# Performance work log

Measured on AMD Instinct MI355X. Metric: run time of the kernel, lower is better.

The kernel has to match this reference:

```python
import jax, jax.numpy as jnp
import numpy as np

DIM = 512
NUM_HEADS = 8
HEAD_DIM = DIM // NUM_HEADS
MAX_SLICES = 1024
SCALE = float(np.sqrt(HEAD_DIM))


def setup_inputs() -> dict:
    key = jax.random.key(0)
    ks = jax.random.split(key, 12)
    B, Nv, Nt, D = 4, 1024, 512, DIM
    std = 0.02
    inp = {
        "visual_tokens": jax.random.normal(ks[0], (B, Nv, D), jnp.float32),
        "text_tokens": jax.random.normal(ks[1], (B, Nt, D), jnp.float32),
        # Linear weights stored as [in, out] (i.e., torch W^T), so y = x @ W + b
        "W_Q": jax.random.normal(ks[2], (D, D), jnp.float32) * std,
        "b_Q": jnp.zeros((D,), jnp.float32),
        "W_K": jax.random.normal(ks[3], (D, D), jnp.float32) * std,
        "b_K": jnp.zeros((D,), jnp.float32),
        "W_V": jax.random.normal(ks[4], (D, D), jnp.float32) * std,
        "b_V": jnp.zeros((D,), jnp.float32),
        "W_O": jax.random.normal(ks[5], (D, D), jnp.float32) * std,
        "b_O": jnp.zeros((D,), jnp.float32),
        "bias_table": jax.random.normal(ks[6], (2 * MAX_SLICES - 1, NUM_HEADS), jnp.float32) * std,
        "ln_gamma": jnp.ones((D,), jnp.float32),
        "ln_beta": jnp.zeros((D,), jnp.float32),
    }
    return inp


def _layernorm(x, gamma, beta, eps=1e-5):
    mu = jnp.mean(x, axis=-1, keepdims=True)
    var = jnp.var(x, axis=-1, keepdims=True)
    return (x - mu) * jax.lax.rsqrt(var + eps) * gamma + beta


def reference(visual_tokens, text_tokens, W_Q, b_Q, W_K, b_K, W_V, b_V, W_O, b_O,
              bias_table, ln_gamma, ln_beta):
    Z = jnp.concatenate([visual_tokens, text_tokens], axis=1)  # [B, N, D]
    B, N, D = Z.shape
    Z = _layernorm(Z, ln_gamma, ln_beta)

    def proj(W, b):
        return (Z @ W + b).reshape(B, N, NUM_HEADS, HEAD_DIM).transpose(0, 2, 1, 3)

    Q = proj(W_Q, b_Q)  # [B, H, N, hd]
    K = proj(W_K, b_K)
    V = proj(W_V, b_V)

    attn = jnp.einsum("bhqd,bhkd->bhqk", Q, K) / SCALE  # [B, H, N, N]

    # relative slice bias: [H, N, N]
    coords = jnp.arange(N)
    rel = coords[:, None] - coords[None, :] + (MAX_SLICES - 1)
    rel = jnp.clip(rel, 0, 2 * MAX_SLICES - 2)
    bias = bias_table[rel]                      # [N, N, H]
    bias = jnp.transpose(bias, (2, 0, 1))[None]  # [1, H, N, N]

    attn = jax.nn.softmax(attn + bias, axis=-1)
    out = jnp.einsum("bhqk,bhkd->bhqd", attn, V)  # [B, H, N, hd]
    out = out.transpose(0, 2, 1, 3).reshape(B, N, D)
    return out @ W_O + b_O
```

## Files before the change

kernel.cpp:

```cpp
#include <hip/hip_runtime.h>
#include <stdint.h>

#define NSEQ   1536
#define NBATCH 4
#define NM     (NBATCH * NSEQ)
#define DMODEL 512
#define NHEAD  8
#define HD     64
#define TBLN   2047

typedef __attribute__((ext_vector_type(4)))  float f32x4;
typedef __attribute__((ext_vector_type(16))) float f32x16;
typedef __attribute__((ext_vector_type(4)))  int   i32x4;
typedef __attribute__((ext_vector_type(2)))  unsigned u32x2;
typedef __attribute__((ext_vector_type(8)))  __bf16 bf16x8;
typedef unsigned short u16;

static_assert(sizeof(bf16x8) == 16, "bf16x8 must be 16B");

__device__ inline u16 f2bf(float f) {
  union { float f; uint32_t u; } v; v.f = f;
  uint32_t u = v.u;
  return (u16)((u + 0x7fffu + ((u >> 16) & 1u)) >> 16);
}

__device__ inline bf16x8 ld_bf8(const u16* p) {
  i32x4 v = *(const i32x4*)p;
  return __builtin_bit_cast(bf16x8, v);
}

__device__ inline f32x4 mfma16(bf16x8 a, bf16x8 b, f32x4 c) {
  return __builtin_amdgcn_mfma_f32_16x16x32_bf16(a, b, c, 0, 0, 0);
}

__device__ inline f32x16 mfma32(bf16x8 a, bf16x8 b, f32x16 c) {
  return __builtin_amdgcn_mfma_f32_32x32x16_bf16(a, b, c, 0, 0, 0);
}

__device__ inline void gload_lds16(const void* g, void* l) {
  __builtin_amdgcn_global_load_lds(
      (__attribute__((address_space(1))) void*)(g),
      (__attribute__((address_space(3))) void*)(l), 16, 0, 0);
}

__device__ inline uint32_t pkbf(float a, float b) {
  uint32_t r;
  asm("v_cvt_pk_bf16_f32 %0, %1, %2" : "=v"(r) : "v"(a), "v"(b));
  return r;
}

__device__ inline void plswap(uint32_t& a, uint32_t& b, int hi) {
#if __has_builtin(__builtin_amdgcn_permlane32_swap)
  u32x2 r = __builtin_amdgcn_permlane32_swap(a, b, false, false);
  a = r[0]; b = r[1];
#else
  const uint32_t as = (uint32_t)__shfl_xor((int)a, 32);
  const uint32_t bs = (uint32_t)__shfl_xor((int)b, 32);
  const uint32_t na = hi ? bs : a;
  const uint32_t nb = hi ? b : as;
  a = na; b = nb;
#endif
}

__device__ inline float exp2_raw(float x) {
  float r;
  asm("v_exp_f32 %0, %1" : "=v"(r) : "v"(x));
  return r;
}

__device__ inline float bfhi(uint32_t u) {
  union { uint32_t u; float f; } v; v.u = u & 0xffff0000u; return v.f;
}
__device__ inline float bflo(uint32_t u) {
  union { uint32_t u; float f; } v; v.u = u << 16; return v.f;
}

__global__ __launch_bounds__(256) void ln_kernel(
    const float* __restrict__ vis, const float* __restrict__ txt,
    const float* __restrict__ gamma, const float* __restrict__ beta,
    u16* __restrict__ zn) {
  const int lane = threadIdx.x & 63;
  const int row  = blockIdx.x * 4 + (threadIdx.x >> 6);
  const int b = row / NSEQ, n = row - b * NSEQ;
  const float* src = (n < 1024) ? (vis + ((size_t)b * 1024 + n) * DMODEL)
                                : (txt + ((size_t)b * 512 + (n - 1024)) * DMODEL);
  const float4* s4 = (const float4*)src;
  float4 x0 = s4[lane], x1 = s4[lane + 64];
  float s = x0.x + x0.y + x0.z + x0.w + x1.x + x1.y + x1.z + x1.w;
  float q = x0.x*x0.x + x0.y*x0.y + x0.z*x0.z + x0.w*x0.w
          + x1.x*x1.x + x1.y*x1.y + x1.z*x1.z + x1.w*x1.w;
  #pragma unroll
  for (int m = 1; m < 64; m <<= 1) { s += __shfl_xor(s, m); q += __shfl_xor(q, m); }
  const float mean = s * (1.0f / 512.0f);
  const float var  = q * (1.0f / 512.0f) - mean * mean;
  const float rstd = rsqrtf(var + 1e-5f);
  const float4* g4 = (const float4*)gamma;
  const float4* b4 = (const float4*)beta;
  float4 g0 = g4[lane], g1 = g4[lane + 64], p0 = b4[lane], p1 = b4[lane + 64];
  u16* dst = zn + (size_t)row * DMODEL;
  ushort4 o0, o1;
  o0.x = f2bf((x0.x - mean) * rstd * g0.x + p0.x);
  o0.y = f2bf((x0.y - mean) * rstd * g0.y + p0.y);
  o0.z = f2bf((x0.z - mean) * rstd * g0.z + p0.z);
  o0.w = f2bf((x0.w - mean) * rstd * g0.w + p0.w);
  o1.x = f2bf((x1.x - mean) * rstd * g1.x + p1.x);
  o1.y = f2bf((x1.y - mean) * rstd * g1.y + p1.y);
  o1.z = f2bf((x1.z - mean) * rstd * g1.z + p1.z);
  o1.w = f2bf((x1.w - mean) * rstd * g1.w + p1.w);
  *(ushort4*)(dst + lane * 4)        = o0;
  *(ushort4*)(dst + (lane + 64) * 4) = o1;
}

__global__ __launch_bounds__(256) void wtrans_kernel(
    const float* __restrict__ WQ, const float* __restrict__ WK,
    const float* __restrict__ WV, const float* __restrict__ WO,
    u16* __restrict__ wqkvt, u16* __restrict__ wot) {
  __shared__ float t[32][33];
  const int m = blockIdx.z;
  const float* W = (m == 0) ? WQ : (m == 1) ? WK : (m == 2) ? WV : WO;
  const int n0 = blockIdx.x * 32, k0 = blockIdx.y * 32;
  const int tx = threadIdx.x & 31, ty = threadIdx.x >> 5;
  #pragma unroll
  for (int j = 0; j < 4; ++j)
    t[ty + j * 8][tx] = W[(size_t)(k0 + ty + j * 8) * DMODEL + n0 + tx];
  __syncthreads();
  u16* out = (m < 3) ? (wqkvt + (size_t)m * DMODEL * DMODEL) : wot;
  #pragma unroll
  for (int j = 0; j < 4; ++j)
    out[(size_t)(n0 + ty + j * 8) * DMODEL + k0 + tx] = f2bf(t[tx][ty + j * 8]);
}

__global__ __launch_bounds__(256) void gemm_qkv(
    const u16* __restrict__ A, const u16* __restrict__ Bt,
    const float* __restrict__ bQ, const float* __restrict__ bK, const float* __restrict__ bV,
    u16* __restrict__ Q, u16* __restrict__ Kk, u16* __restrict__ Vt) {
  __shared__ __align__(16) u16 lat[128 * 64];
  __shared__ __align__(16) u16 lbt[96 * 64];
  const int tid = threadIdx.x, lane = tid & 63, w = tid >> 6;
  const int wr = w >> 1, wc = w & 1;
  const int m0 = blockIdx.y * 128, n0 = blockIdx.x * 96;
  f32x4 acc[4][3] = {};
  for (int kt = 0; kt < 8; ++kt) {
    const int k0 = kt * 64;
    #pragma unroll
    for (int i = 0; i < 4; ++i) {
      int ch = tid + 256 * i;
      int row = ch >> 3, pc = ch & 7;
      int kk = k0 + ((pc ^ (row & 7)) << 3);
      gload_lds16(A + (size_t)(m0 + row) * DMODEL + kk, lat + (size_t)ch * 8);
    }
    #pragma unroll
    for (int i = 0; i < 3; ++i) {
      int ch = tid + 256 * i;
      int row = ch >> 3, pc = ch & 7;
      int kk = k0 + ((pc ^ (row & 7)) << 3);
      gload_lds16(Bt + (size_t)(n0 + row) * DMODEL + kk, lbt + (size_t)ch * 8);
    }
    __syncthreads();
    #pragma unroll
    for (int ks = 0; ks < 2; ++ks) {
      bf16x8 af[4], bfr[3];
      const int cc = ks * 4 + (lane >> 4);
      #pragma unroll
      for (int f = 0; f < 4; ++f) {
        int ra = wr * 64 + f * 16 + (lane & 15);
        af[f]  = ld_bf8(lat + ra * 64 + ((cc ^ (ra & 7)) << 3));
      }
      #pragma unroll
      for (int f = 0; f < 3; ++f) {
        int rb = wc * 48 + f * 16 + (lane & 15);
        bfr[f] = ld_bf8(lbt + rb * 64 + ((cc ^ (rb & 7)) << 3));
      }
      #pragma unroll
      for (int fr = 0; fr < 4; ++fr)
        #pragma unroll
        for (int fc = 0; fc < 3; ++fc)
          acc[fr][fc] = mfma16(af[fr], bfr[fc], acc[fr][fc]);
    }
    __syncthreads();
  }
  #pragma unroll
  for (int fr = 0; fr < 4; ++fr) {
    const int mbase = m0 + wr * 64 + fr * 16 + ((lane >> 4) << 2);
    const int b = mbase / NSEQ;
    const int nseq = mbase - b * NSEQ;
    #pragma unroll
    for (int fc = 0; fc < 3; ++fc) {
      const int col = n0 + wc * 48 + fc * 16 + (lane & 15);
      const int which = col >> 9;
      const int cw = col & 511;
      const int h = cw >> 6, d = cw & 63;
      const float bias = (which == 0) ? bQ[cw] : (which == 1) ? bK[cw] : bV[cw];
      if (which < 2) {
        u16* dst = ((which == 0) ? Q : Kk) + ((size_t)(b * NHEAD + h) * NSEQ + nseq) * HD + d;
        #pragma unroll
        for (int r = 0; r < 4; ++r) dst[(size_t)r * HD] = f2bf(acc[fr][fc][r] + bias);
      } else {
        ushort4 pv;
        pv.x = f2bf(acc[fr][fc][0] + bias);
        pv.y = f2bf(acc[fr][fc][1] + bias);
        pv.z = f2bf(acc[fr][fc][2] + bias);
        pv.w = f2bf(acc[fr][fc][3] + bias);
        *(ushort4*)(Vt + ((size_t)(b * NHEAD + h) * HD + d) * NSEQ + nseq) = pv;
      }
    }
  }
}

__global__ __launch_bounds__(256) void gemm_oproj(
    const u16* __restrict__ A, const u16* __restrict__ Bt,
    const float* __restrict__ bO, float* __restrict__ out) {
  __shared__ __align__(16) u16 lat[64 * 64];
  __shared__ __align__(16) u16 lbt[64 * 64];
  const int tid = threadIdx.x, lane = tid & 63, w = tid >> 6;
  const int wr = w >> 1, wc = w & 1;
  const int m0 = blockIdx.y * 64, n0 = blockIdx.x * 64;
  f32x4 acc[2][2] = {};
  for (int kt = 0; kt < 8; ++kt) {
    const int k0 = kt * 64;
    #pragma unroll
    for (int i = 0; i < 2; ++i) {
      int ch = tid + 256 * i;
      int row = ch >> 3, pc = ch & 7;
      int kk = k0 + ((pc ^ (row & 7)) << 3);
      gload_lds16(A  + (size_t)(m0 + row) * DMODEL + kk, lat + (size_t)ch * 8);
      gload_lds16(Bt + (size_t)(n0 + row) * DMODEL + kk, lbt + (size_t)ch * 8);
    }
    __syncthreads();
    #pragma unroll
    for (int ks = 0; ks < 2; ++ks) {
      bf16x8 af[2], bfr[2];
      const int cc = ks * 4 + (lane >> 4);
      #pragma unroll
      for (int f = 0; f < 2; ++f) {
        int ra = wr * 32 + f * 16 + (lane & 15);
        af[f]  = ld_bf8(lat + ra * 64 + ((cc ^ (ra & 7)) << 3));
        int rb = wc * 32 + f * 16 + (lane & 15);
        bfr[f] = ld_bf8(lbt + rb * 64 + ((cc ^ (rb & 7)) << 3));
      }
      #pragma unroll
      for (int fr = 0; fr < 2; ++fr)
        #pragma unroll
        for (int fc = 0; fc < 2; ++fc)
          acc[fr][fc] = mfma16(af[fr], bfr[fc], acc[fr][fc]);
    }
    __syncthreads();
  }
  #pragma unroll
  for (int fr = 0; fr < 2; ++fr) {
    const int mbase = m0 + wr * 32 + fr * 16 + ((lane >> 4) << 2);
    #pragma unroll
    for (int fc = 0; fc < 2; ++fc) {
      const int col = n0 + wc * 32 + fc * 16 + (lane & 15);
      const float bias = bO[col];
      float* dst = out + (size_t)mbase * DMODEL + col;
      #pragma unroll
      for (int r = 0; r < 4; ++r) dst[(size_t)r * DMODEL] = acc[fr][fc][r] + bias;
    }
  }
}

__global__ __launch_bounds__(768, 3) void attn_kernel(
    const u16* __restrict__ Q, const u16* __restrict__ K,
    const u16* __restrict__ Vt, const float* __restrict__ table,
    u16* __restrict__ O) {
  __shared__ __align__(16) char smem[77824];
  u16* rb2k = (u16*)smem;
  const int tid = threadIdx.x, lane = tid & 63, w = tid >> 6;
  const int bid = blockIdx.x;
  const int xcd = bid & 7, idx = bid >> 3;
  const int bh  = xcd * 4 + (idx & 3);
  const int qt  = idx >> 2;
  const int h   = bh & (NHEAD - 1);
  for (int t = tid; t < 2 * 3072; t += 768) {
    const int c = (t >= 3072) ? 1 : 0;
    const int x = t - c * 3072;
    int src = 2558 - (x + c);
    src = src < 0 ? 0 : (src > 2046 ? 2046 : src);
    rb2k[c * 3072 + x] = f2bf(table[(size_t)src * NHEAD + h] * 1.4426950408889634f);
  }

  const int lo32 = lane & 31, hi = lane >> 5;
  const int ws = (w < 6) ? w : (w - 6);
  const int hf = (w < 6) ? 0 : 1;
  const int kbase = hf * 768;
  const int q  = qt * 192 + ws * 32 + lo32;
  const u16* Qb = Q  + (size_t)bh * NSEQ * HD;
  const u16* Kb = K  + (size_t)bh * NSEQ * HD;
  const u16* Vb = Vt + (size_t)bh * HD * NSEQ;

  const int tloc = tid - hf * 384;
  u16* kl0 = (u16*)(smem + 12288) + hf * 2 * 4096;
  u16* vl0 = (u16*)(smem + 45056) + hf * 2 * 4096;
#define STAGE(b, k0loc)                                                       \
  if (tloc < 256) {                                                           \
    _Pragma("unroll")                                                         \
    for (int i = 0; i < 2; ++i) {                                             \
      int ch = tloc + 256 * i;                                                \
      int row = ch >> 3, pc = ch & 7;                                         \
      int col = (pc ^ (row & 7)) << 3;                                        \
      gload_lds16(Kb + (size_t)(kbase + (k0loc) + row) * HD + col,            \
                  kl0 + (size_t)(b) * 4096 + ch * 8);                         \
      gload_lds16(Vb + (size_t)row * NSEQ + kbase + (k0loc) + col,            \
                  vl0 + (size_t)(b) * 4096 + ch * 8);                         \
    }                                                                         \
  }

  bf16x8 qf[4];
  #pragma unroll
  for (int ds = 0; ds < 4; ++ds)
    qf[ds] = ld_bf8(Qb + (size_t)q * HD + ds * 16 + hi * 8);

  float l_part = 0.f;
  f32x16 acc[2] = {};

  const int rswz = lo32 & 7;
  const int T0  = 1535 - q + 4 * hi + kbase;
  const int c2  = T0 & 1;
  const int dwb = (T0 - c2) >> 1;
  const uint32_t* rbp32 = (const uint32_t*)(rb2k + c2 * 3072);
  const float c1 = 0.125f * 1.4426950408889634f;

  STAGE(0, 0);
  __syncthreads();
  int cur = 0;

  for (int kt = 0; kt < 12; ++kt) {
    const int nxt = cur ^ 1;
    if (kt < 11) {
      STAGE(nxt, (kt + 1) * 64);
      asm volatile("s_waitcnt vmcnt(4)" ::: "memory");
    } else {
      asm volatile("s_waitcnt vmcnt(0)" ::: "memory");
    }
    __builtin_amdgcn_s_barrier();
    const u16* kb = (u16*)(smem + 12288) + (hf * 2 + cur) * 4096;
    const u16* vb = (u16*)(smem + 45056) + (hf * 2 + cur) * 4096;
    #pragma unroll
    for (int ktile = 0; ktile < 2; ++ktile) {
      f32x16 st = {};
      __builtin_amdgcn_s_setprio(1);
      #pragma unroll
      for (int ds = 0; ds < 4; ++ds) {
        const int row = ktile * 32 + lo32;
        const bf16x8 kf = ld_bf8(kb + row * 64 + (((2 * ds + hi) ^ rswz) << 3));
        st = mfma32(kf, qf[ds], st);
      }
      __builtin_amdgcn_s_setprio(0);
      const int dwk = dwb + ((kt * 64 + ktile * 32) >> 1);
      float bv[4][4];
      #pragma unroll
      for (int gp = 0; gp < 4; ++gp) {
        const uint32_t u0 = rbp32[dwk + 4 * gp];
        const uint32_t u1 = rbp32[dwk + 4 * gp + 1];
        bv[gp][0] = bflo(u0); bv[gp][1] = bfhi(u0);
        bv[gp][2] = bflo(u1); bv[gp][3] = bfhi(u1);
      }
      #pragma unroll
      for (int r = 0; r < 16; ++r) {
        float p = exp2_raw(__builtin_fmaf(st[r], c1, bv[r >> 2][r & 3]));
        st[r] = p;
        l_part += p;
      }
      uint32_t wv[8];
      #pragma unroll
      for (int i = 0; i < 8; ++i) wv[i] = pkbf(st[2 * i], st[2 * i + 1]);
      plswap(wv[0], wv[2], hi);  plswap(wv[1], wv[3], hi);
      plswap(wv[4], wv[6], hi);  plswap(wv[5], wv[7], hi);
      i32x4 b0; b0[0] = (int)wv[0]; b0[1] = (int)wv[1]; b0[2] = (int)wv[2]; b0[3] = (int)wv[3];
      i32x4 b1; b1[0] = (int)wv[4]; b1[1] = (int)wv[5]; b1[2] = (int)wv[6]; b1[3] = (int)wv[7];
      const bf16x8 pb0 = __builtin_bit_cast(bf16x8, b0);
      const bf16x8 pb1 = __builtin_bit_cast(bf16x8, b1);
      __builtin_amdgcn_s_setprio(1);
      #pragma unroll
      for (int dh = 0; dh < 2; ++dh) {
        const int vrow = dh * 32 + lo32;
        const bf16x8 va0 = ld_bf8(vb + vrow * 64 + (((4 * ktile + 0 + hi) ^ rswz) << 3));
        acc[dh] = mfma32(va0, pb0, acc[dh]);
        const bf16x8 va1 = ld_bf8(vb + vrow * 64 + (((4 * ktile + 2 + hi) ^ rswz) << 3));
        acc[dh] = mfma32(va1, pb1, acc[dh]);
      }
      __builtin_amdgcn_s_setprio(0);
    }
    __builtin_amdgcn_s_barrier();
    cur = nxt;
  }
  float* scr = (float*)(smem + 12288);
  if (hf == 1) {
    float* wb = scr + ws * 2112;
    #pragma unroll
    for (int dh = 0; dh < 2; ++dh)
      #pragma unroll
      for (int i = 0; i < 4; ++i) {
        f32x4 c4; c4[0] = acc[dh][4*i]; c4[1] = acc[dh][4*i+1];
        c4[2] = acc[dh][4*i+2]; c4[3] = acc[dh][4*i+3];
        ((f32x4*)wb)[(dh * 4 + i) * 64 + lane] = c4;
      }
    wb[2048 + lane] = l_part;
  }
  __syncthreads();
  if (hf == 0) {
    const float* rb = scr + ws * 2112;
    #pragma unroll
    for (int dh = 0; dh < 2; ++dh)
      #pragma unroll
      for (int i = 0; i < 4; ++i) {
        const f32x4 c4 = ((const f32x4*)rb)[(dh * 4 + i) * 64 + lane];
        acc[dh][4*i] += c4[0]; acc[dh][4*i+1] += c4[1];
        acc[dh][4*i+2] += c4[2]; acc[dh][4*i+3] += c4[3];
      }
    l_part += rb[2048 + lane];
    float l_r = l_part + __shfl_xor(l_part, 32);
    const float inv = 1.0f / l_r;
    const int b = bh >> 3;
    u16* orow = O + ((size_t)(b * NSEQ + q)) * DMODEL + h * HD;
    #pragma unroll
    for (int dh = 0; dh < 2; ++dh)
      #pragma unroll
      for (int gp = 0; gp < 4; ++gp) {
        uint2 o4;
        o4.x = pkbf(acc[dh][4*gp]   * inv, acc[dh][4*gp+1] * inv);
        o4.y = pkbf(acc[dh][4*gp+2] * inv, acc[dh][4*gp+3] * inv);
        *(uint2*)(orow + dh * 32 + 8 * gp + 4 * hi) = o4;
      }
  }
#undef STAGE
}

extern "C" void kernel_launch(void* const* d_in, const int* in_sizes, int n_in,
                              void* d_out, int out_size, void* d_ws, size_t ws_size,
                              hipStream_t stream) {
  const float* vis   = (const float*)d_in[0];
  const float* txt   = (const float*)d_in[1];
  const float* WQ    = (const float*)d_in[2];
  const float* bQ    = (const float*)d_in[3];
  const float* WK    = (const float*)d_in[4];
  const float* bK    = (const float*)d_in[5];
  const float* WV    = (const float*)d_in[6];
  const float* bV    = (const float*)d_in[7];
  const float* WO    = (const float*)d_in[8];
  const float* bO    = (const float*)d_in[9];
  const float* table = (const float*)d_in[10];
  const float* gamma = (const float*)d_in[11];
  const float* beta  = (const float*)d_in[12];
  float* out = (float*)d_out;

  char* p = (char*)d_ws;
  u16* zn    = (u16*)p; p += (size_t)NM * DMODEL * 2;
  u16* wqkvt = (u16*)p; p += (size_t)3 * DMODEL * DMODEL * 2;
  u16* wot   = (u16*)p; p += (size_t)DMODEL * DMODEL * 2;
  u16* q     = (u16*)p; p += (size_t)NM * DMODEL * 2;
  u16* k     = (u16*)p; p += (size_t)NM * DMODEL * 2;
  u16* vt    = (u16*)p; p += (size_t)NM * DMODEL * 2;
  u16* o     = (u16*)p; p += (size_t)NM * DMODEL * 2;

  hipLaunchKernelGGL(ln_kernel, dim3(NM / 4), dim3(256), 0, stream,
                     vis, txt, gamma, beta, zn);
  hipLaunchKernelGGL(wtrans_kernel, dim3(16, 16, 4), dim3(256), 0, stream,
                     WQ, WK, WV, WO, wqkvt, wot);
  hipLaunchKernelGGL(gemm_qkv, dim3(16, 48), dim3(256), 0, stream,
                     zn, wqkvt, bQ, bK, bV, q, k, vt);
  hipLaunchKernelGGL(attn_kernel, dim3(256), dim3(768), 0, stream,
                     q, k, vt, table, o);
  hipLaunchKernelGGL(gemm_oproj, dim3(8, 96), dim3(256), 0, stream,
                     o, wot, bO, out);
}
```

Baseline: 81.99 us.

## Double-buffer LDS in projection GEMMs with larger M tiles and MFMA priority

Both projection GEMMs (QKV and output) now keep two LDS stages, prefetching the next K tile while MFMAs run on the current one. They use partial vmcnt waits and raw barriers in place of the two full syncthreads per iteration. M tiles grow from 128 to 192 and from 64 to 96 rows, with matching grid shrinkage, and s_setprio raises wave priority around the MFMA blocks. The aim is to hide global-to-LDS latency and amortise the B-tile loads. The cost is more LDS and registers per block, which may cut occupancy, and fewer blocks in the grid.

Measured after the change: 75.44 us. 8.0% less time.

```diff
diff --git a/kernel.cpp b/kernel.cpp
--- a/kernel.cpp
+++ b/kernel.cpp
@@ -130,58 +130,74 @@
     out[(size_t)(n0 + ty + j * 8) * DMODEL + k0 + tx] = f2bf(t[tx][ty + j * 8]);
 }
 
-__global__ __launch_bounds__(256) void gemm_qkv(
+__global__ __launch_bounds__(256, 2) void gemm_qkv(
     const u16* __restrict__ A, const u16* __restrict__ Bt,
     const float* __restrict__ bQ, const float* __restrict__ bK, const float* __restrict__ bV,
     u16* __restrict__ Q, u16* __restrict__ Kk, u16* __restrict__ Vt) {
-  __shared__ __align__(16) u16 lat[128 * 64];
-  __shared__ __align__(16) u16 lbt[96 * 64];
+  __shared__ __align__(16) u16 lat[2][192 * 64];
+  __shared__ __align__(16) u16 lbt[2][96 * 64];
   const int tid = threadIdx.x, lane = tid & 63, w = tid >> 6;
   const int wr = w >> 1, wc = w & 1;
-  const int m0 = blockIdx.y * 128, n0 = blockIdx.x * 96;
-  f32x4 acc[4][3] = {};
+  const int m0 = blockIdx.y * 192, n0 = blockIdx.x * 96;
+  f32x4 acc[6][3] = {};
+#define QSTAGE(buf, k0)                                                        \
+  do {                                                                         \
+    _Pragma("unroll")                                                          \
+    for (int i = 0; i < 6; ++i) {                                              \
+      int ch = tid + 256 * i;                              \
+      int row = ch >> 3, pc = ch & 7;                                          \
+      int kk = (k0) + ((pc ^ (row & 7)) << 3);                                 \
+      gload_lds16(A + (size_t)(m0 + row) * DMODEL + kk, lat[buf] + (size_t)ch * 8); \
+    }                                                                          \
+    _Pragma("unroll")                                                          \
+    for (int i = 0; i < 3; ++i) {                                              \
+      int ch = tid + 256 * i;                               \
+      int row = ch >> 3, pc = ch & 7;                                          \
+      int kk = (k0) + ((pc ^ (row & 7)) << 3);                                 \
+      gload_lds16(Bt + (size_t)(n0 + row) * DMODEL + kk, lbt[buf] + (size_t)ch * 8); \
+    }                                                                          \
+  } while (0)
+
+  QSTAGE(0, 0);
+  __syncthreads();
+  int cur = 0;
   for (int kt = 0; kt < 8; ++kt) {
-    const int k0 = kt * 64;
-    #pragma unroll
-    for (int i = 0; i < 4; ++i) {
-      int ch = tid + 256 * i;
-      int row = ch >> 3, pc = ch & 7;
-      int kk = k0 + ((pc ^ (row & 7)) << 3);
-      gload_lds16(A + (size_t)(m0 + row) * DMODEL + kk, lat + (size_t)ch * 8);
-    }
-    #pragma unroll
-    for (int i = 0; i < 3; ++i) {
-      int ch = tid + 256 * i;
-      int row = ch >> 3, pc = ch & 7;
-      int kk = k0 + ((pc ^ (row & 7)) << 3);
-      gload_lds16(Bt + (size_t)(n0 + row) * DMODEL + kk, lbt + (size_t)ch * 8);
-    }
-    __syncthreads();
+    const int nxt = cur ^ 1;
+    if (kt < 7) {
+      QSTAGE(nxt, (kt + 1) * 64);
+      asm volatile("s_waitcnt vmcnt(9)" ::: "memory");
+    } else {
+      asm volatile("s_waitcnt vmcnt(0)" ::: "memory");
+    }
+    __builtin_amdgcn_s_barrier();
     #pragma unroll
     for (int ks = 0; ks < 2; ++ks) {
-      bf16x8 af[4], bfr[3];
+      bf16x8 af[6], bfr[3];
       const int cc = ks * 4 + (lane >> 4);
       #pragma unroll
-      for (int f = 0; f < 4; ++f) {
-        int ra = wr * 64 + f * 16 + (lane & 15);
-        af[f]  = ld_bf8(lat + ra * 64 + ((cc ^ (ra & 7)) << 3));
+      for (int f = 0; f < 6; ++f) {
+        int ra = wr * 96 + f * 16 + (lane & 15);
+        af[f]  = ld_bf8(lat[cur] + ra * 64 + ((cc ^ (ra & 7)) << 3));
       }
       #pragma unroll
       for (int f = 0; f < 3; ++f) {
         int rb = wc * 48 + f * 16 + (lane & 15);
-        bfr[f] = ld_bf8(lbt + rb * 64 + ((cc ^ (rb & 7)) << 3));
-      }
-      #pragma unroll
-      for (int fr = 0; fr < 4; ++fr)
+        bfr[f] = ld_bf8(lbt[cur] + rb * 64 + ((cc ^ (rb & 7)) << 3));
+      }
+      __builtin_amdgcn_s_setprio(1);
+      #pragma unroll
+      for (int fr = 0; fr < 6; ++fr)
         #pragma unroll
         for (int fc = 0; fc < 3; ++fc)
           acc[fr][fc] = mfma16(af[fr], bfr[fc], acc[fr][fc]);
-    }
-    __syncthreads();
+      __builtin_amdgcn_s_setprio(0);
+    }
+    __builtin_amdgcn_s_barrier();
+    cur = nxt;
   }
   #pragma unroll
-  for (int fr = 0; fr < 4; ++fr) {
-    const int mbase = m0 + wr * 64 + fr * 16 + ((lane >> 4) << 2);
+  for (int fr = 0; fr < 6; ++fr) {
+    const int mbase = m0 + wr * 96 + fr * 16 + ((lane >> 4) << 2);
     const int b = mbase / NSEQ;
     const int nseq = mbase - b * NSEQ;
     #pragma unroll
@@ -205,50 +221,76 @@
       }
     }
   }
-}
-
-__global__ __launch_bounds__(256) void gemm_oproj(
+#undef QSTAGE
+}
+
+__global__ __launch_bounds__(256, 2) void gemm_oproj(
     const u16* __restrict__ A, const u16* __restrict__ Bt,
     const float* __restrict__ bO, float* __restrict__ out) {
-  __shared__ __align__(16) u16 lat[64 * 64];
-  __shared__ __align__(16) u16 lbt[64 * 64];
+  __shared__ __align__(16) u16 lat[2][96 * 64];
+  __shared__ __align__(16) u16 lbt[2][64 * 64];
   const int tid = threadIdx.x, lane = tid & 63, w = tid >> 6;
   const int wr = w >> 1, wc = w & 1;
-  const int m0 = blockIdx.y * 64, n0 = blockIdx.x * 64;
-  f32x4 acc[2][2] = {};
+  const int m0 = blockIdx.y * 96, n0 = blockIdx.x * 64;
+  f32x4 acc[3][2] = {};
+#define OSTAGE(buf, k0)                                                        \
+  do {                                                                         \
+    _Pragma("unroll")                                                          \
+    for (int i = 0; i < 3; ++i) {                                              \
+      int ch = tid + 256 * i;                               \
+      int row = ch >> 3, pc = ch & 7;                                          \
+      int kk = (k0) + ((pc ^ (row & 7)) << 3);                                 \
+      gload_lds16(A + (size_t)(m0 + row) * DMODEL + kk, lat[buf] + (size_t)ch * 8); \
+    }                                                                          \
+    _Pragma("unroll")                                                          \
+    for (int i = 0; i < 2; ++i) {                                              \
+      int ch = tid + 256 * i;                               \
+      int row = ch >> 3, pc = ch & 7;                                          \
+      int kk = (k0) + ((pc ^ (row & 7)) << 3);                                 \
+      gload_lds16(Bt + (size_t)(n0 + row) * DMODEL + kk, lbt[buf] + (size_t)ch * 8); \
+    }                                                                          \
+  } while (0)
+
+  OSTAGE(0, 0);
+  __syncthreads();
+  int cur = 0;
   for (int kt = 0; kt < 8; ++kt) {
-    const int k0 = kt * 64;
-    #pragma unroll
-    for (int i = 0; i < 2; ++i) {
-      int ch = tid + 256 * i;
-      int row = ch >> 3, pc = ch & 7;
-      int kk = k0 + ((pc ^ (row & 7)) << 3);
-      gload_lds16(A  + (size_t)(m0 + row) * DMODEL + kk, lat + (size_t)ch * 8);
-      gload_lds16(Bt + (size_t)(n0 + row) * DMODEL + kk, lbt + (size_t)ch * 8);
-    }
-    __syncthreads();
+    const int nxt = cur ^ 1;
+    if (kt < 7) {
+      OSTAGE(nxt, (kt + 1) * 64);
+      asm volatile("s_waitcnt vmcnt(5)" ::: "memory");
+    } else {
+      asm volatile("s_waitcnt vmcnt(0)" ::: "memory");
+    }
+    __builtin_amdgcn_s_barrier();
     #pragma unroll
     for (int ks = 0; ks < 2; ++ks) {
-      bf16x8 af[2], bfr[2];
+      bf16x8 af[3], bfr[2];
       const int cc = ks * 4 + (lane >> 4);
       #pragma unroll
+      for (int f = 0; f < 3; ++f) {
+        int ra = wr * 48 + f * 16 + (lane & 15);
+        af[f]  = ld_bf8(lat[cur] + ra * 64 + ((cc ^ (ra & 7)) << 3));
+      }
+      #pragma unroll
       for (int f = 0; f < 2; ++f) {
-        int ra = wr * 32 + f * 16 + (lane & 15);
-        af[f]  = ld_bf8(lat + ra * 64 + ((cc ^ (ra & 7)) << 3));
         int rb = wc * 32 + f * 16 + (lane & 15);
-        bfr[f] = ld_bf8(lbt + rb * 64 + ((cc ^ (rb & 7)) << 3));
-      }
-      #pragma unroll
-      for (int fr = 0; fr < 2; ++fr)
+        bfr[f] = ld_bf8(lbt[cur] + rb * 64 + ((cc ^ (rb & 7)) << 3));
+      }
+      __builtin_amdgcn_s_setprio(1);
+      #pragma unroll
+      for (int fr = 0; fr < 3; ++fr)
         #pragma unroll
         for (int fc = 0; fc < 2; ++fc)
           acc[fr][fc] = mfma16(af[fr], bfr[fc], acc[fr][fc]);
-    }
-    __syncthreads();
+      __builtin_amdgcn_s_setprio(0);
+    }
+    __builtin_amdgcn_s_barrier();
+    cur = nxt;
   }
   #pragma unroll
-  for (int fr = 0; fr < 2; ++fr) {
-    const int mbase = m0 + wr * 32 + fr * 16 + ((lane >> 4) << 2);
+  for (int fr = 0; fr < 3; ++fr) {
+    const int mbase = m0 + wr * 48 + fr * 16 + ((lane >> 4) << 2);
     #pragma unroll
     for (int fc = 0; fc < 2; ++fc) {
       const int col = n0 + wc * 32 + fc * 16 + (lane & 15);
@@ -258,6 +300,7 @@
       for (int r = 0; r < 4; ++r) dst[(size_t)r * DMODEL] = acc[fr][fc][r] + bias;
     }
   }
+#undef OSTAGE
 }
 
 __global__ __launch_bounds__(768, 3) void attn_kernel(
@@ -458,10 +501,10 @@
                      vis, txt, gamma, beta, zn);
   hipLaunchKernelGGL(wtrans_kernel, dim3(16, 16, 4), dim3(256), 0, stream,
                      WQ, WK, WV, WO, wqkvt, wot);
-  hipLaunchKernelGGL(gemm_qkv, dim3(16, 48), dim3(256), 0, stream,
+  hipLaunchKernelGGL(gemm_qkv, dim3(16, 32), dim3(256), 0, stream,
                      zn, wqkvt, bQ, bK, bV, q, k, vt);
   hipLaunchKernelGGL(attn_kernel, dim3(256), dim3(768), 0, stream,
                      q, k, vt, table, o);
-  hipLaunchKernelGGL(gemm_oproj, dim3(8, 96), dim3(256), 0, stream,
+  hipLaunchKernelGGL(gemm_oproj, dim3(8, 64), dim3(256), 0, stream,
                      o, wot, bO, out);
 }
```
